# Optimization experiments

Hardware: AMD Instinct MI355X
Metric: run time of the kernel (lower is better)

## Reference

```python
import jax, jax.numpy as jnp
import numpy as np

EPS = 1e-12  # F.normalize eps


def _l2norm(x):
    n = jnp.sqrt(jnp.sum(x * x, axis=-1, keepdims=True))
    return x / jnp.maximum(n, EPS)


def setup_inputs() -> dict:
    key = jax.random.key(0)
    k1, k2, k3 = jax.random.split(key, 3)
    B, C, D = 512, 100000, 128
    batch = jax.random.normal(k1, (B, D), dtype=jnp.float32)
    labels = jax.random.randint(k2, (B,), 0, C, dtype=jnp.int64)
    proxies = jax.random.normal(k3, (C, D), dtype=jnp.float32) / 8
    return {"batch": batch, "labels": labels, "proxies": proxies}


def reference(batch, labels, proxies):
    # batch: [B, D], labels: [B] int, proxies: [C, D]
    x = 3.0 * _l2norm(batch)          # [B, D]
    p = 3.0 * _l2norm(proxies)        # [C, D]
    x2 = jnp.sum(x * x, axis=1, keepdims=True)       # [B, 1]
    p2 = jnp.sum(p * p, axis=1)[None, :]             # [1, C]
    dist = x2 + p2 - 2.0 * jnp.einsum("bd,cd->bc", x, p)  # [B, C]
    B = batch.shape[0]
    pos_dist = dist[jnp.arange(B), labels]           # [B]
    # logsumexp(-dist) over negatives only: mask out positive class
    is_pos = labels[:, None] == jnp.arange(proxies.shape[0])[None, :]  # [B, C]
    neg_scores = jnp.where(is_pos, -jnp.inf, -dist)
    neg_lse = jax.nn.logsumexp(neg_scores, axis=1)   # [B]
    return jnp.mean(pos_dist + neg_lse)
```

## Files before the change

kernel.cpp:

```cpp
#include <hip/hip_runtime.h>
#include <hip/hip_bf16.h>
#include <math.h>

#define B_ 512
#define C_ 100000
#define D_ 128
#define SC 64
#define NSTEP ((C_ + SC - 1) / SC)
#define NPAD (NSTEP * SC - C_)
#define GRID_MAIN 256
#define LOG2E 1.4426950408889634f
#define K2S (2.0f * LOG2E)
#define K18S (-18.0f * LOG2E)

typedef __attribute__((ext_vector_type(8))) short short8;
typedef __attribute__((ext_vector_type(4))) float f32x4;

__device__ __forceinline__ float b2f(unsigned short u) {
  union { float f; unsigned int i; } v; v.i = ((unsigned int)u) << 16; return v.f;
}

#if defined(__has_builtin)
#if __has_builtin(__builtin_amdgcn_exp2f)
#define EXP2F(x) __builtin_amdgcn_exp2f(x)
#endif
#endif
#ifndef EXP2F
#define EXP2F(x) __expf(0.69314718055994531f * (x))
#endif

__device__ __forceinline__ void gll16(const void* g, void* l) {
  __builtin_amdgcn_global_load_lds(
      (const __attribute__((address_space(1))) void*)g,
      (__attribute__((address_space(3))) void*)l, 16, 0, 0);
}

__global__ __launch_bounds__(512, 2) void pnca_main_kernel(
    const float* __restrict__ praw, const float* __restrict__ batch,
    float* __restrict__ pt)
{
  __shared__ __align__(16) float         fbuf[2][SC * D_];
  __shared__ __align__(16) unsigned char bbuf[2][SC * D_ * 2];

  const int tid  = threadIdx.x;
  const int lane = tid & 63;
  const int w    = tid >> 6;
  const int ll   = lane & 15;
  const int lq   = lane >> 4;
  const int st0  = blockIdx.x;

  short8 a[4][4];
#pragma unroll
  for (int m = 0; m < 4; ++m) {
    float4 t0[4], t1[4];
    float ssm = 0.f;
#pragma unroll
    for (int ks = 0; ks < 4; ++ks) {
      const float* rp = batch + (size_t)(w * 64 + m * 16 + ll) * D_ + ks * 32 + lq * 8;
      t0[ks] = *(const float4*)rp;
      t1[ks] = *(const float4*)(rp + 4);
      ssm += t0[ks].x * t0[ks].x + t0[ks].y * t0[ks].y + t0[ks].z * t0[ks].z + t0[ks].w * t0[ks].w
           + t1[ks].x * t1[ks].x + t1[ks].y * t1[ks].y + t1[ks].z * t1[ks].z + t1[ks].w * t1[ks].w;
    }
    ssm += __shfl_xor(ssm, 16);
    ssm += __shfl_xor(ssm, 32);
    float sc = 3.f / fmaxf(sqrtf(ssm), 1e-12f);
#pragma unroll
    for (int ks = 0; ks < 4; ++ks) {
      union { short8 s8; __hip_bfloat162 h[4]; } u;
      u.h[0] = __float22bfloat162_rn(make_float2(t0[ks].x * sc, t0[ks].y * sc));
      u.h[1] = __float22bfloat162_rn(make_float2(t0[ks].z * sc, t0[ks].w * sc));
      u.h[2] = __float22bfloat162_rn(make_float2(t1[ks].x * sc, t1[ks].y * sc));
      u.h[3] = __float22bfloat162_rn(make_float2(t1[ks].z * sc, t1[ks].w * sc));
      a[m][ks] = u.s8;
    }
  }
  asm volatile("s_waitcnt vmcnt(0)" ::: "memory");

  float part[4][4];
#pragma unroll
  for (int m = 0; m < 4; ++m)
#pragma unroll
    for (int r = 0; r < 4; ++r) part[m][r] = 0.f;

  auto STAGE = [&](int st, int pp) {
    const unsigned char* gb = (const unsigned char*)praw;
#pragma unroll
    for (int k = 0; k < 4; ++k) {
      int slot = k * 512 + tid;
      int gr   = st * SC + (slot >> 5);
      if (gr >= C_) gr = C_ - 1;
      gll16(gb + ((size_t)gr * 32 + (slot & 31)) * 16,
            (unsigned char*)fbuf[pp] + (size_t)(k * 512 + w * 64) * 16);
    }
  };

  auto CVT = [&](int st, int pp) {
    const int c = tid >> 3, j = tid & 7;
    const float* Fb = fbuf[pp] + (size_t)c * D_;
    float x[16]; float ss = 0.f;
#pragma unroll
    for (int i = 0; i < 4; ++i) {
      float4 v = *(const float4*)(Fb + (j + 8 * i) * 4);
      x[4*i+0] = v.x; x[4*i+1] = v.y; x[4*i+2] = v.z; x[4*i+3] = v.w;
      ss += v.x * v.x + v.y * v.y + v.z * v.z + v.w * v.w;
    }
    ss += __shfl_xor(ss, 1);
    ss += __shfl_xor(ss, 2);
    ss += __shfl_xor(ss, 4);
    float sc = (st * SC + c < C_) ? 3.0f * __frsqrt_rn(fmaxf(ss, 1e-24f)) : 0.0f;
    unsigned char* Bb = bbuf[pp];
#pragma unroll
    for (int i = 0; i < 4; ++i) {
      union { unsigned long long q; __hip_bfloat162 h[2]; } u2;
      u2.h[0] = __float22bfloat162_rn(make_float2(x[4*i]   * sc, x[4*i+1] * sc));
      u2.h[1] = __float22bfloat162_rn(make_float2(x[4*i+2] * sc, x[4*i+3] * sc));
      int lu = (j >> 1) + 4 * i;
      int pu = lu ^ (c & 7);
      *(unsigned long long*)(Bb + ((size_t)c * 16 + pu) * 16 + (j & 1) * 8) = u2.q;
    }
  };

  auto COMPUTE = [&](int pp) {
    const unsigned char* Bb = bbuf[pp];
#pragma unroll
    for (int g = 0; g < 4; ++g) {
      const int cg = g * 16 + ll;
      short8 bfr[4];
#pragma unroll
      for (int ks = 0; ks < 4; ++ks)
        bfr[ks] = *(const short8*)(Bb + (size_t)(cg * 16 + ((ks * 4 + lq) ^ (cg & 7))) * 16);
      f32x4 acc[4];
#pragma unroll
      for (int m = 0; m < 4; ++m) acc[m] = (f32x4){0.f, 0.f, 0.f, 0.f};
#pragma unroll
      for (int ks = 0; ks < 4; ++ks)
#pragma unroll
        for (int m = 0; m < 4; ++m)
          acc[m] = __builtin_amdgcn_mfma_f32_16x16x32_bf16(a[m][ks], bfr[ks], acc[m], 0, 0, 0);
#pragma unroll
      for (int m = 0; m < 4; ++m)
#pragma unroll
        for (int r = 0; r < 4; ++r)
          part[m][r] += EXP2F(fmaf(acc[m][r], K2S, K18S));
    }
  };

  STAGE(st0, 0);
  STAGE(st0 + GRID_MAIN, 1);
  asm volatile("s_waitcnt vmcnt(4)" ::: "memory");
  __builtin_amdgcn_s_barrier();
  __builtin_amdgcn_sched_barrier(0);
  CVT(st0, 0);
  __builtin_amdgcn_s_barrier();

  int cur = 0;
  for (int st = st0; st < NSTEP; st += GRID_MAIN) {
    const int s1 = st + GRID_MAIN;
    const int s2 = st + 2 * GRID_MAIN;
    const bool h1 = (s1 < NSTEP);
    const bool h2 = (s2 < NSTEP);
    if (h2) STAGE(s2, cur);
    if (h1) {
      if (h2) asm volatile("s_waitcnt vmcnt(4)" ::: "memory");
      else    asm volatile("s_waitcnt vmcnt(0)" ::: "memory");
    }
    __builtin_amdgcn_s_barrier();
    __builtin_amdgcn_sched_barrier(0);
    if (h1) CVT(s1, cur ^ 1);
    COMPUTE(cur);
    __builtin_amdgcn_s_barrier();
    cur ^= 1;
  }

#pragma unroll
  for (int m = 0; m < 4; ++m)
#pragma unroll
    for (int r = 0; r < 4; ++r) {
      float v = part[m][r];
      v += __shfl_xor(v, 1);
      v += __shfl_xor(v, 2);
      v += __shfl_xor(v, 4);
      v += __shfl_xor(v, 8);
      if (ll == 0)
        pt[(size_t)blockIdx.x * B_ + w * 64 + m * 16 + lq * 4 + r] = v;
    }
}

__global__ __launch_bounds__(256) void finalize_rows_kernel(
    const float* __restrict__ praw, const float* __restrict__ batch,
    const int* __restrict__ labels, const float* __restrict__ pt,
    float* __restrict__ lossb)
{
  int lane = threadIdx.x & 63, wv = threadIdx.x >> 6;
  int row = blockIdx.x * 4 + wv;
  int lab = labels[row];
  float2 pv = *(const float2*)(praw + (size_t)lab * D_ + lane * 2);
  float2 xv = *(const float2*)(batch + (size_t)row * D_ + lane * 2);
  float ssp = pv.x * pv.x + pv.y * pv.y;
  float ssx = xv.x * xv.x + xv.y * xv.y;
  float dp  = xv.x * pv.x + xv.y * pv.y;
#pragma unroll
  for (int off = 32; off; off >>= 1) {
    ssp += __shfl_xor(ssp, off);
    ssx += __shfl_xor(ssx, off);
    dp  += __shfl_xor(dp, off);
  }
  float pd = 18.f - 18.f * dp / (fmaxf(sqrtf(ssx), 1e-12f) * fmaxf(sqrtf(ssp), 1e-12f));
  float s = 0.f;
#pragma unroll
  for (int gg = 0; gg < GRID_MAIN / 64; ++gg)
    s += pt[(size_t)(gg * 64 + lane) * B_ + row];
#pragma unroll
  for (int off = 32; off; off >>= 1) s += __shfl_xor(s, off);
  if (lane == 0) {
    const float tail = (float)NPAD * EXP2F(K18S);
    lossb[row] = pd + logf(s - __expf(-pd) - tail);
  }
}

__global__ __launch_bounds__(512) void reduce_mean_kernel(
    const float* __restrict__ lossb, float* __restrict__ out)
{
  int t = threadIdx.x;
  float v = lossb[t];
#pragma unroll
  for (int off = 1; off < 64; off <<= 1) v += __shfl_xor(v, off);
  __shared__ float red[8];
  if ((t & 63) == 0) red[t >> 6] = v;
  __syncthreads();
  if (t == 0) {
    float tot = 0.f;
    for (int i = 0; i < 8; ++i) tot += red[i];
    out[0] = tot / (float)B_;
  }
}

extern "C" void kernel_launch(void* const* d_in, const int* in_sizes, int n_in,
                              void* d_out, int out_size, void* d_ws, size_t ws_size,
                              hipStream_t stream)
{
  const float* batch   = (const float*)d_in[0];
  const int*   labels  = (const int*)d_in[1];
  const float* proxies = (const float*)d_in[2];
  float* out = (float*)d_out;

  unsigned char* ws = (unsigned char*)d_ws;
  float* pt    = (float*)ws;
  float* lossb = (float*)(ws + (size_t)GRID_MAIN * B_ * 4);

  pnca_main_kernel<<<GRID_MAIN, 512, 0, stream>>>(proxies, batch, pt);
  finalize_rows_kernel<<<B_ / 4, 256, 0, stream>>>(proxies, batch, labels, pt, lossb);
  reduce_mean_kernel<<<1, 512, 0, stream>>>(lossb, out);
}
```

Baseline: 40.54 us.

## Split batch rows across grid Y and use smaller contiguous proxy tiles per block

Reworks the main kernel decomposition: the batch is split into two 256-row halves on grid Y, and proxy tiles shrink to 32 rows. Each block now processes 6 contiguous tiles over 521×2 blocks, replacing the previous strided loop over 256 blocks. The aim is higher occupancy (4 blocks per CU, smaller LDS and register footprint) and better load balance across CUs. In exchange every proxy tile is loaded and normalized twice, once per batch half. The explicit vmcnt pipelining is also replaced with plain __syncthreads, which may expose load latency.

```diff
diff --git a/kernel.cpp b/kernel.cpp
--- a/kernel.cpp
+++ b/kernel.cpp
@@ -5,20 +5,16 @@
 #define B_ 512
 #define C_ 100000
 #define D_ 128
-#define SC 64
-#define NSTEP ((C_ + SC - 1) / SC)
-#define NPAD (NSTEP * SC - C_)
-#define GRID_MAIN 256
+#define SC 32
+#define NITER 6
+#define GX 521
+#define NPAD (GX * NITER * SC - C_)
 #define LOG2E 1.4426950408889634f
 #define K2S (2.0f * LOG2E)
 #define K18S (-18.0f * LOG2E)
 
 typedef __attribute__((ext_vector_type(8))) short short8;
 typedef __attribute__((ext_vector_type(4))) float f32x4;
-
-__device__ __forceinline__ float b2f(unsigned short u) {
-  union { float f; unsigned int i; } v; v.i = ((unsigned int)u) << 16; return v.f;
-}
 
 #if defined(__has_builtin)
 #if __has_builtin(__builtin_amdgcn_exp2f)
@@ -35,28 +31,30 @@
       (__attribute__((address_space(3))) void*)l, 16, 0, 0);
 }
 
-__global__ __launch_bounds__(512, 2) void pnca_main_kernel(
+__global__ __launch_bounds__(512, 4) void pnca_main_kernel(
     const float* __restrict__ praw, const float* __restrict__ batch,
     float* __restrict__ pt)
 {
   __shared__ __align__(16) float         fbuf[2][SC * D_];
-  __shared__ __align__(16) unsigned char bbuf[2][SC * D_ * 2];
+  __shared__ __align__(16) unsigned char bbuf[2][SC * 256];
 
   const int tid  = threadIdx.x;
   const int lane = tid & 63;
   const int w    = tid >> 6;
   const int ll   = lane & 15;
   const int lq   = lane >> 4;
-  const int st0  = blockIdx.x;
-
-  short8 a[4][4];
-#pragma unroll
-  for (int m = 0; m < 4; ++m) {
+  const int gx   = blockIdx.x;
+  const int st0  = gx * NITER;
+  const int rb   = blockIdx.y * 256;
+
+  short8 a[2][4];
+#pragma unroll
+  for (int m = 0; m < 2; ++m) {
     float4 t0[4], t1[4];
     float ssm = 0.f;
 #pragma unroll
     for (int ks = 0; ks < 4; ++ks) {
-      const float* rp = batch + (size_t)(w * 64 + m * 16 + ll) * D_ + ks * 32 + lq * 8;
+      const float* rp = batch + (size_t)(rb + w * 32 + m * 16 + ll) * D_ + ks * 32 + lq * 8;
       t0[ks] = *(const float4*)rp;
       t1[ks] = *(const float4*)(rp + 4);
       ssm += t0[ks].x * t0[ks].x + t0[ks].y * t0[ks].y + t0[ks].z * t0[ks].z + t0[ks].w * t0[ks].w
@@ -75,18 +73,17 @@
       a[m][ks] = u.s8;
     }
   }
-  asm volatile("s_waitcnt vmcnt(0)" ::: "memory");
-
-  float part[4][4];
-#pragma unroll
-  for (int m = 0; m < 4; ++m)
+
+  float part[2][4];
+#pragma unroll
+  for (int m = 0; m < 2; ++m)
 #pragma unroll
     for (int r = 0; r < 4; ++r) part[m][r] = 0.f;
 
   auto STAGE = [&](int st, int pp) {
     const unsigned char* gb = (const unsigned char*)praw;
 #pragma unroll
-    for (int k = 0; k < 4; ++k) {
+    for (int k = 0; k < 2; ++k) {
       int slot = k * 512 + tid;
       int gr   = st * SC + (slot >> 5);
       if (gr >= C_) gr = C_ - 1;
@@ -96,85 +93,71 @@
   };
 
   auto CVT = [&](int st, int pp) {
-    const int c = tid >> 3, j = tid & 7;
-    const float* Fb = fbuf[pp] + (size_t)c * D_;
-    float x[16]; float ss = 0.f;
-#pragma unroll
-    for (int i = 0; i < 4; ++i) {
-      float4 v = *(const float4*)(Fb + (j + 8 * i) * 4);
-      x[4*i+0] = v.x; x[4*i+1] = v.y; x[4*i+2] = v.z; x[4*i+3] = v.w;
-      ss += v.x * v.x + v.y * v.y + v.z * v.z + v.w * v.w;
-    }
+    const int c = tid >> 4, j = tid & 15;
+    const float* Fb = fbuf[pp] + (size_t)c * D_ + j * 8;
+    float4 v0 = *(const float4*)Fb;
+    float4 v1 = *(const float4*)(Fb + 4);
+    float ss = v0.x * v0.x + v0.y * v0.y + v0.z * v0.z + v0.w * v0.w
+             + v1.x * v1.x + v1.y * v1.y + v1.z * v1.z + v1.w * v1.w;
     ss += __shfl_xor(ss, 1);
     ss += __shfl_xor(ss, 2);
     ss += __shfl_xor(ss, 4);
+    ss += __shfl_xor(ss, 8);
     float sc = (st * SC + c < C_) ? 3.0f * __frsqrt_rn(fmaxf(ss, 1e-24f)) : 0.0f;
-    unsigned char* Bb = bbuf[pp];
-#pragma unroll
-    for (int i = 0; i < 4; ++i) {
-      union { unsigned long long q; __hip_bfloat162 h[2]; } u2;
-      u2.h[0] = __float22bfloat162_rn(make_float2(x[4*i]   * sc, x[4*i+1] * sc));
-      u2.h[1] = __float22bfloat162_rn(make_float2(x[4*i+2] * sc, x[4*i+3] * sc));
-      int lu = (j >> 1) + 4 * i;
-      int pu = lu ^ (c & 7);
-      *(unsigned long long*)(Bb + ((size_t)c * 16 + pu) * 16 + (j & 1) * 8) = u2.q;
-    }
+    union { short8 s8; __hip_bfloat162 h[4]; } u;
+    u.h[0] = __float22bfloat162_rn(make_float2(v0.x * sc, v0.y * sc));
+    u.h[1] = __float22bfloat162_rn(make_float2(v0.z * sc, v0.w * sc));
+    u.h[2] = __float22bfloat162_rn(make_float2(v1.x * sc, v1.y * sc));
+    u.h[3] = __float22bfloat162_rn(make_float2(v1.z * sc, v1.w * sc));
+    int pu = j ^ (c & 7);
+    *(short8*)(bbuf[pp] + (size_t)c * 256 + pu * 16) = u.s8;
   };
 
   auto COMPUTE = [&](int pp) {
     const unsigned char* Bb = bbuf[pp];
 #pragma unroll
-    for (int g = 0; g < 4; ++g) {
+    for (int g = 0; g < 2; ++g) {
       const int cg = g * 16 + ll;
       short8 bfr[4];
 #pragma unroll
       for (int ks = 0; ks < 4; ++ks)
-        bfr[ks] = *(const short8*)(Bb + (size_t)(cg * 16 + ((ks * 4 + lq) ^ (cg & 7))) * 16);
-      f32x4 acc[4];
-#pragma unroll
-      for (int m = 0; m < 4; ++m) acc[m] = (f32x4){0.f, 0.f, 0.f, 0.f};
-#pragma unroll
-      for (int ks = 0; ks < 4; ++ks)
-#pragma unroll
-        for (int m = 0; m < 4; ++m)
-          acc[m] = __builtin_amdgcn_mfma_f32_16x16x32_bf16(a[m][ks], bfr[ks], acc[m], 0, 0, 0);
-#pragma unroll
-      for (int m = 0; m < 4; ++m)
-#pragma unroll
-        for (int r = 0; r < 4; ++r)
-          part[m][r] += EXP2F(fmaf(acc[m][r], K2S, K18S));
+        bfr[ks] = *(const short8*)(Bb + (size_t)cg * 256 + ((ks * 4 + lq) ^ (cg & 7)) * 16);
+      f32x4 acc0 = (f32x4){0.f, 0.f, 0.f, 0.f};
+      f32x4 acc1 = (f32x4){0.f, 0.f, 0.f, 0.f};
+#pragma unroll
+      for (int ks = 0; ks < 4; ++ks) {
+        acc0 = __builtin_amdgcn_mfma_f32_16x16x32_bf16(a[0][ks], bfr[ks], acc0, 0, 0, 0);
+        acc1 = __builtin_amdgcn_mfma_f32_16x16x32_bf16(a[1][ks], bfr[ks], acc1, 0, 0, 0);
+      }
+#pragma unroll
+      for (int r = 0; r < 4; ++r) {
+        part[0][r] += EXP2F(fmaf(acc0[r], K2S, K18S));
+        part[1][r] += EXP2F(fmaf(acc1[r], K2S, K18S));
+      }
     }
   };
 
   STAGE(st0, 0);
-  STAGE(st0 + GRID_MAIN, 1);
-  asm volatile("s_waitcnt vmcnt(4)" ::: "memory");
-  __builtin_amdgcn_s_barrier();
-  __builtin_amdgcn_sched_barrier(0);
+  __syncthreads();
   CVT(st0, 0);
-  __builtin_amdgcn_s_barrier();
-
-  int cur = 0;
-  for (int st = st0; st < NSTEP; st += GRID_MAIN) {
-    const int s1 = st + GRID_MAIN;
-    const int s2 = st + 2 * GRID_MAIN;
-    const bool h1 = (s1 < NSTEP);
-    const bool h2 = (s2 < NSTEP);
-    if (h2) STAGE(s2, cur);
-    if (h1) {
-      if (h2) asm volatile("s_waitcnt vmcnt(4)" ::: "memory");
-      else    asm volatile("s_waitcnt vmcnt(0)" ::: "memory");
-    }
-    __builtin_amdgcn_s_barrier();
-    __builtin_amdgcn_sched_barrier(0);
-    if (h1) CVT(s1, cur ^ 1);
-    COMPUTE(cur);
-    __builtin_amdgcn_s_barrier();
-    cur ^= 1;
-  }
-
-#pragma unroll
-  for (int m = 0; m < 4; ++m)
+  __syncthreads();
+
+  int p = 0;
+#pragma unroll
+  for (int it = 0; it < NITER; ++it) {
+    const bool hn = (it + 1 < NITER);
+    if (hn) STAGE(st0 + it + 1, p ^ 1);
+    COMPUTE(p);
+    if (hn) {
+      __syncthreads();
+      CVT(st0 + it + 1, p ^ 1);
+      __syncthreads();
+    }
+    p ^= 1;
+  }
+
+#pragma unroll
+  for (int m = 0; m < 2; ++m)
 #pragma unroll
     for (int r = 0; r < 4; ++r) {
       float v = part[m][r];
@@ -183,7 +166,7 @@
       v += __shfl_xor(v, 4);
       v += __shfl_xor(v, 8);
       if (ll == 0)
-        pt[(size_t)blockIdx.x * B_ + w * 64 + m * 16 + lq * 4 + r] = v;
+        pt[(size_t)gx * B_ + rb + w * 32 + m * 16 + lq * 4 + r] = v;
     }
 }
 
@@ -208,9 +191,7 @@
   }
   float pd = 18.f - 18.f * dp / (fmaxf(sqrtf(ssx), 1e-12f) * fmaxf(sqrtf(ssp), 1e-12f));
   float s = 0.f;
-#pragma unroll
-  for (int gg = 0; gg < GRID_MAIN / 64; ++gg)
-    s += pt[(size_t)(gg * 64 + lane) * B_ + row];
+  for (int gg = lane; gg < GX; gg += 64) s += pt[(size_t)gg * B_ + row];
 #pragma unroll
   for (int off = 32; off; off >>= 1) s += __shfl_xor(s, off);
   if (lane == 0) {
@@ -247,9 +228,10 @@
 
   unsigned char* ws = (unsigned char*)d_ws;
   float* pt    = (float*)ws;
-  float* lossb = (float*)(ws + (size_t)GRID_MAIN * B_ * 4);
-
-  pnca_main_kernel<<<GRID_MAIN, 512, 0, stream>>>(proxies, batch, pt);
+  float* lossb = (float*)(ws + (size_t)GX * B_ * 4);
+
+  dim3 grid(GX, 2);
+  pnca_main_kernel<<<grid, 512, 0, stream>>>(proxies, batch, pt);
   finalize_rows_kernel<<<B_ / 4, 256, 0, stream>>>(proxies, batch, labels, pt, lossb);
   reduce_mean_kernel<<<1, 512, 0, stream>>>(lossb, out);
 }
```

New measurement: 70.67 us. 74.3% more time.
